# Kernel optimization log

Measured on AMD Instinct MI355X. Metric: run time of the kernel, lower is better.

## Reference

```python
import jax, jax.numpy as jnp
import numpy as np

N, E = 20000, 320000
IN_F, H, D = 1280, 4, 128
HD = H * D  # 512
NEG_SLOPE = 0.2


def setup_inputs() -> dict:
    key = jax.random.key(0)
    ks = jax.random.split(key, 16)
    feature = jax.random.normal(ks[0], (1, N, IN_F), dtype=jnp.float32)
    src = jax.random.randint(ks[1], (E,), 0, N, dtype=jnp.int32)
    dst = jnp.sort(jax.random.randint(ks[2], (E,), 0, N, dtype=jnp.int32))
    s1 = 1.0 / np.sqrt(IN_F)
    s2 = 1.0 / np.sqrt(HD)
    W1 = jax.random.normal(ks[3], (IN_F, HD), dtype=jnp.float32) * s1
    al1 = jax.random.normal(ks[4], (H, D), dtype=jnp.float32) * s2
    ar1 = jax.random.normal(ks[5], (H, D), dtype=jnp.float32) * s2
    b1 = jnp.zeros((HD,), dtype=jnp.float32)
    W2 = jax.random.normal(ks[6], (HD, HD), dtype=jnp.float32) * s2
    al2 = jax.random.normal(ks[7], (H, D), dtype=jnp.float32) * s2
    ar2 = jax.random.normal(ks[8], (H, D), dtype=jnp.float32) * s2
    b2 = jnp.zeros((HD,), dtype=jnp.float32)
    Wfc = jax.random.normal(ks[9], (HD, 64), dtype=jnp.float32) * s2
    bfc = jnp.zeros((64,), dtype=jnp.float32)
    return dict(feature=feature, src=src, dst=dst, W1=W1, al1=al1, ar1=ar1,
                b1=b1, W2=W2, al2=al2, ar2=ar2, b2=b2, Wfc=Wfc, bfc=bfc)


def gat_conv(x, src, dst, W, al, ar, b):
    # x: (N, F_in) -> (N, H, D). DGL GATConv math, negative_slope=0.2.
    h = (x @ W).reshape(N, H, D)
    el = jnp.sum(h * al, axis=-1)                       # (N, H)
    er = jnp.sum(h * ar, axis=-1)                       # (N, H)
    e = jax.nn.leaky_relu(el[src] + er[dst], NEG_SLOPE)  # (E, H)
    # edge softmax segmented by destination node
    m = jax.ops.segment_max(e, dst, num_segments=N, indices_are_sorted=True)
    ex = jnp.exp(e - m[dst])                            # (E, H)
    denom = jax.ops.segment_sum(ex, dst, num_segments=N, indices_are_sorted=True)
    alpha = ex / denom[dst]                             # (E, H)
    out = jax.ops.segment_sum(alpha[:, :, None] * h[src], dst,
                              num_segments=N, indices_are_sorted=True)  # (N,H,D)
    return out + b.reshape(H, D)


def reference(feature, src, dst, W1, al1, ar1, b1, W2, al2, ar2, b2, Wfc, bfc):
    x = feature[0]                                      # squeeze(0) -> (N, 1280)
    out = gat_conv(x, src, dst, W1, al1, ar1, b1)
    out = jax.nn.elu(out).reshape(N, HD)
    out = gat_conv(out, src, dst, W2, al2, ar2, b2)
    out = jax.nn.elu(out).reshape(N, HD)
    out = out @ Wfc + bfc                               # (N, 64)
    out = jax.nn.elu(out[None])                         # (1, N, 64)
    return out
```

## Files before the change

### kernel.cpp

```cpp
#include <hip/hip_runtime.h>
#include <hip/hip_bf16.h>
#include <math.h>
#include <type_traits>

typedef __bf16 bf16_t;
typedef __bf16 bf16x8 __attribute__((ext_vector_type(8)));
typedef float f32x4 __attribute__((ext_vector_type(4)));

__device__ __forceinline__ void gload_lds16(const void* g, void* l) {
  __builtin_amdgcn_global_load_lds((const __attribute__((address_space(1))) void*)g,
                                   (__attribute__((address_space(3))) void*)l, 16, 0, 0);
}

__global__ void transk(const float* __restrict__ in, bf16_t* __restrict__ out,
                       int K, int N) {
  __shared__ float t[32][33];
  int n0 = blockIdx.x * 32, k0 = blockIdx.y * 32;
  int tx = threadIdx.x & 31, ty = threadIdx.x >> 5;
#pragma unroll
  for (int r = ty; r < 32; r += 8) t[r][tx] = in[(size_t)(k0 + r) * N + n0 + tx];
  __syncthreads();
#pragma unroll
  for (int r = ty; r < 32; r += 8)
    out[(size_t)(n0 + r) * K + k0 + tx] = (bf16_t)t[tx][r];
}

__global__ void rowoffk(const int* __restrict__ dst, int* __restrict__ ro, int N, int E) {
  int n = blockIdx.x * blockDim.x + threadIdx.x;
  if (n > N) return;
  if (n == N) { ro[N] = E; return; }
  int lo = 0, hi = E;
  while (lo < hi) { int mid = (lo + hi) >> 1; if (dst[mid] < n) lo = mid + 1; else hi = mid; }
  ro[n] = lo;
}

__global__ void elerk(const bf16_t* __restrict__ Hb, const float* __restrict__ al,
                      const float* __restrict__ ar, float* __restrict__ el,
                      float* __restrict__ er, int N) {
  int node = blockIdx.x * 4 + (threadIdx.x >> 6);
  int lane = threadIdx.x & 63;
  if (node >= N) return;
  bf16x8 v = *(const bf16x8*)(Hb + (size_t)node * 512 + lane * 8);
  int head = lane >> 4;
  int dbase = (lane & 15) * 8;
  float sl = 0.f, sr = 0.f;
#pragma unroll
  for (int t = 0; t < 8; t++) {
    float f = (float)v[t];
    sl += f * al[head * 128 + dbase + t];
    sr += f * ar[head * 128 + dbase + t];
  }
#pragma unroll
  for (int off = 1; off < 16; off <<= 1) {
    sl += __shfl_xor(sl, off);
    sr += __shfl_xor(sr, off);
  }
  if ((lane & 15) == 0) {
    el[node * 4 + head] = sl;
    er[node * 4 + head] = sr;
  }
}

__global__ void edgek(const float* __restrict__ el, const float* __restrict__ er,
                      const int* __restrict__ src, const int* __restrict__ dst,
                      float* __restrict__ pw, int E) {
  int e = blockIdx.x * blockDim.x + threadIdx.x;
  if (e >= E) return;
  int s = src[e], d = dst[e];
  float4 ev = *(const float4*)(el + (size_t)s * 4);
  float4 rv = *(const float4*)(er + (size_t)d * 4);
  float c;
  c = ev.x + rv.x; c = c >= 0.f ? c : 0.2f * c; pw[e] = __expf(c);
  c = ev.y + rv.y; c = c >= 0.f ? c : 0.2f * c; pw[(size_t)E + e] = __expf(c);
  c = ev.z + rv.z; c = c >= 0.f ? c : 0.2f * c; pw[(size_t)2 * E + e] = __expf(c);
  c = ev.w + rv.w; c = c >= 0.f ? c : 0.2f * c; pw[(size_t)3 * E + e] = __expf(c);
}

#define GK_NPB 32
__global__ __launch_bounds__(256) void gatherk(
    const bf16_t* __restrict__ Hb, const float* __restrict__ pw,
    const int* __restrict__ src, const int* __restrict__ ro,
    const float* __restrict__ bias, bf16_t* __restrict__ out, int N, int E) {
  const int slice = blockIdx.x & 7;
  const int group = blockIdx.x >> 3;
  const int w = threadIdx.x >> 6, lane = threadIdx.x & 63;
  const int g = lane >> 3;
  const int oct = lane & 7;
  const int head = slice >> 1;
  const float* __restrict__ ph = pw + (size_t)head * E;
  const int dimbase = slice * 64 + oct * 8;

  const int n = group * GK_NPB + w * 8 + g;
  const int e0 = ro[n], e1 = ro[n + 1];

  float acc[8] = {0.f, 0.f, 0.f, 0.f, 0.f, 0.f, 0.f, 0.f};
  float psum = 0.f;

  for (int eb = e0 & ~7; eb < e1; eb += 8) {
    const int4 sv0 = *(const int4*)(src + eb);
    const int4 sv1 = *(const int4*)(src + eb + 4);
    const float4 pv0 = *(const float4*)(ph + eb);
    const float4 pv1 = *(const float4*)(ph + eb + 4);
    int ss[8]; float pp[8];
    ss[0] = sv0.x; ss[1] = sv0.y; ss[2] = sv0.z; ss[3] = sv0.w;
    ss[4] = sv1.x; ss[5] = sv1.y; ss[6] = sv1.z; ss[7] = sv1.w;
    pp[0] = pv0.x; pp[1] = pv0.y; pp[2] = pv0.z; pp[3] = pv0.w;
    pp[4] = pv1.x; pp[5] = pv1.y; pp[6] = pv1.z; pp[7] = pv1.w;
#pragma unroll
    for (int j = 0; j < 8; j++) {
      const int e = eb + j;
      if (e < e0 || e >= e1) pp[j] = 0.f;
    }
    bf16x8 v[8];
#pragma unroll
    for (int j = 0; j < 8; j++)
      v[j] = *(const bf16x8*)(Hb + (size_t)ss[j] * 512 + dimbase);
#pragma unroll
    for (int j = 0; j < 8; j++) {
      psum += pp[j];
#pragma unroll
      for (int t = 0; t < 8; t++) acc[t] += pp[j] * (float)v[j][t];
    }
  }

  const float ih = psum > 0.f ? 1.0f / psum : 0.f;
  const float4 b0 = *(const float4*)(bias + dimbase);
  const float4 b1 = *(const float4*)(bias + dimbase + 4);
  bf16x8 o; float vv;
  vv = acc[0] * ih + b0.x; o[0] = (bf16_t)(vv > 0.f ? vv : expm1f(vv));
  vv = acc[1] * ih + b0.y; o[1] = (bf16_t)(vv > 0.f ? vv : expm1f(vv));
  vv = acc[2] * ih + b0.z; o[2] = (bf16_t)(vv > 0.f ? vv : expm1f(vv));
  vv = acc[3] * ih + b0.w; o[3] = (bf16_t)(vv > 0.f ? vv : expm1f(vv));
  vv = acc[4] * ih + b1.x; o[4] = (bf16_t)(vv > 0.f ? vv : expm1f(vv));
  vv = acc[5] * ih + b1.y; o[5] = (bf16_t)(vv > 0.f ? vv : expm1f(vv));
  vv = acc[6] * ih + b1.z; o[6] = (bf16_t)(vv > 0.f ? vv : expm1f(vv));
  vv = acc[7] * ih + b1.w; o[7] = (bf16_t)(vv > 0.f ? vv : expm1f(vv));
  *(bf16x8*)(out + (size_t)n * 512 + dimbase) = o;
}

template <int BM, int BN, int WM, int WN, int EPI, int AF32>
__global__ __launch_bounds__(256) void gemm_bt(
    const void* __restrict__ A, const bf16_t* __restrict__ Bt,
    void* __restrict__ C, const float* __restrict__ bias,
    int M, int N, int K) {
  constexpr int BK = 32;
  constexpr int WTM = BM / WM, WTN = BN / WN;
  constexpr int MF = WTM / 16, NF = WTN / 16;
  using AT = typename std::conditional<AF32, float, bf16_t>::type;

  __shared__ AT sA[BM][BK];
  __shared__ bf16_t sB[BN][BK];

  const bf16_t* __restrict__ Ab = (const bf16_t*)A;
  const float* __restrict__ Af = (const float*)A;

  const int tid = threadIdx.x;
  const int wid = tid >> 6, lane = tid & 63;
  const int wr = wid / WN, wc = wid % WN;

  const int nby = N / BN;
  const int nwg = gridDim.x;
  const int q = nwg >> 3, r = nwg & 7;
  const int xcd = blockIdx.x & 7, pos = blockIdx.x >> 3;
  const int wg = (xcd < r ? xcd * (q + 1) : r * (q + 1) + (xcd - r) * q) + pos;
  const int row0 = (wg / nby) * BM;
  const int col0 = (wg % nby) * BN;

  f32x4 acc[MF][NF];
#pragma unroll
  for (int i = 0; i < MF; i++)
#pragma unroll
    for (int j = 0; j < NF; j++) acc[i][j] = (f32x4){0.f, 0.f, 0.f, 0.f};

  const int lr = lane >> 2;
  const int lkb = (lane & 3) * 8;
  const int a_lr = lane >> 3;
  const int a_seg = (lane & 7) ^ (lane >> 3);

  for (int k0 = 0; k0 < K; k0 += BK) {
    if constexpr (AF32) {
#pragma unroll
      for (int j = 0; j < BM / 32; j++) {
        const int rj = (j * 4 + wid) * 8;
        int grow = row0 + rj + a_lr; if (grow > M - 1) grow = M - 1;
        gload_lds16(Af + (size_t)grow * K + k0 + a_seg * 4, &sA[rj][0]);
      }
    } else {
#pragma unroll
      for (int i = 0; i < BM / 16; i += 4) {
        int r2 = (i + wid) * 16 + lr;
        int grow = row0 + r2; if (grow > M - 1) grow = M - 1;
        gload_lds16(Ab + (size_t)grow * K + k0 + lkb, &sA[(i + wid) * 16][0]);
      }
    }
#pragma unroll
    for (int i = 0; i < BN / 16; i += 4) {
      int r2 = (i + wid) * 16 + lr;
      gload_lds16(Bt + (size_t)(col0 + r2) * K + k0 + lkb, &sB[(i + wid) * 16][0]);
    }
    __syncthreads();
    bf16x8 af[MF], bfr[NF];
#pragma unroll
    for (int i = 0; i < MF; i++) {
      const int row = wr * WTM + i * 16 + (lane & 15);
      if constexpr (AF32) {
        const int h = lane >> 4;
        const int rowm = row & 7;
        const int p0 = (2 * h) ^ rowm, p1 = (2 * h + 1) ^ rowm;
        const f32x4 a0 = *(const f32x4*)&((const float*)&sA[row][0])[p0 * 4];
        const f32x4 a1 = *(const f32x4*)&((const float*)&sA[row][0])[p1 * 4];
#pragma unroll
        for (int t = 0; t < 4; t++) {
          af[i][t] = (bf16_t)a0[t];
          af[i][t + 4] = (bf16_t)a1[t];
        }
      } else {
        af[i] = *(const bf16x8*)&((const bf16_t*)&sA[row][0])[(lane >> 4) * 8];
      }
    }
#pragma unroll
    for (int j = 0; j < NF; j++)
      bfr[j] = *(const bf16x8*)&sB[wc * WTN + j * 16 + (lane & 15)][(lane >> 4) * 8];
#pragma unroll
    for (int i = 0; i < MF; i++)
#pragma unroll
      for (int j = 0; j < NF; j++)
        acc[i][j] = __builtin_amdgcn_mfma_f32_16x16x32_bf16(af[i], bfr[j], acc[i][j], 0, 0, 0);
    __syncthreads();
  }

#pragma unroll
  for (int i = 0; i < MF; i++) {
#pragma unroll
    for (int j = 0; j < NF; j++) {
#pragma unroll
      for (int rr = 0; rr < 4; rr++) {
        int row = row0 + wr * WTM + i * 16 + (lane >> 4) * 4 + rr;
        int col = col0 + wc * WTN + j * 16 + (lane & 15);
        if (row < M) {
          float v = acc[i][j][rr];
          if constexpr (EPI == 0) {
            ((bf16_t*)C)[(size_t)row * N + col] = (bf16_t)v;
          } else {
            v += bias[col];
            v = v > 0.f ? v : expm1f(v);
            ((float*)C)[(size_t)row * N + col] = v;
          }
        }
      }
    }
  }
}

extern "C" void kernel_launch(void* const* d_in, const int* in_sizes, int n_in,
                              void* d_out, int out_size, void* d_ws, size_t ws_size,
                              hipStream_t stream) {
  const float* feature = (const float*)d_in[0];
  const int* src = (const int*)d_in[1];
  const int* dst = (const int*)d_in[2];
  const float* W1 = (const float*)d_in[3];
  const float* al1 = (const float*)d_in[4];
  const float* ar1 = (const float*)d_in[5];
  const float* b1 = (const float*)d_in[6];
  const float* W2 = (const float*)d_in[7];
  const float* al2 = (const float*)d_in[8];
  const float* ar2 = (const float*)d_in[9];
  const float* b2 = (const float*)d_in[10];
  const float* Wfc = (const float*)d_in[11];
  const float* bfc = (const float*)d_in[12];

  const int N = 20000, E = 320000, INF = 1280, HD = 512;

  char* ws = (char*)d_ws;
  size_t off = 0;
  auto alloc = [&](size_t bytes) {
    void* p = ws + off;
    off += (bytes + 255) & ~(size_t)255;
    return p;
  };
  bf16_t* W1t = (bf16_t*)alloc((size_t)HD * INF * 2);
  bf16_t* W2t = (bf16_t*)alloc((size_t)HD * HD * 2);
  bf16_t* Wft = (bf16_t*)alloc((size_t)64 * HD * 2);
  bf16_t* Hb  = (bf16_t*)alloc((size_t)N * HD * 2);
  bf16_t* Xn  = (bf16_t*)alloc((size_t)N * HD * 2);
  float* el = (float*)alloc((size_t)N * 4 * 4);
  float* er = (float*)alloc((size_t)N * 4 * 4);
  float* pw = (float*)alloc((size_t)E * 4 * 4);
  int* ro = (int*)alloc((size_t)(N + 1) * 4);

  {
    dim3 g(HD / 32, INF / 32);
    transk<<<g, 256, 0, stream>>>(W1, W1t, INF, HD);
  }
  {
    dim3 g(HD / 32, HD / 32);
    transk<<<g, 256, 0, stream>>>(W2, W2t, HD, HD);
  }
  {
    dim3 g(64 / 32, HD / 32);
    transk<<<g, 256, 0, stream>>>(Wfc, Wft, HD, 64);
  }
  rowoffk<<<(N + 1 + 255) / 256, 256, 0, stream>>>(dst, ro, N, E);

  const int nbx = (N + 127) / 128;
  const int gatherBlocks = (N / GK_NPB) * 8;
  const int edgeBlocks = (E + 255) / 256;

  gemm_bt<128, 128, 2, 2, 0, 1><<<nbx * (HD / 128), 256, 0, stream>>>(
      feature, W1t, Hb, nullptr, N, HD, INF);
  elerk<<<N / 4, 256, 0, stream>>>(Hb, al1, ar1, el, er, N);
  edgek<<<edgeBlocks, 256, 0, stream>>>(el, er, src, dst, pw, E);
  gatherk<<<gatherBlocks, 256, 0, stream>>>(Hb, pw, src, ro, b1, Xn, N, E);

  gemm_bt<128, 128, 2, 2, 0, 0><<<nbx * (HD / 128), 256, 0, stream>>>(
      Xn, W2t, Hb, nullptr, N, HD, HD);
  elerk<<<N / 4, 256, 0, stream>>>(Hb, al2, ar2, el, er, N);
  edgek<<<edgeBlocks, 256, 0, stream>>>(el, er, src, dst, pw, E);
  gatherk<<<gatherBlocks, 256, 0, stream>>>(Hb, pw, src, ro, b2, Xn, N, E);

  gemm_bt<128, 64, 4, 1, 1, 0><<<nbx, 256, 0, stream>>>(Xn, Wft, d_out, bfc, N, 64, HD);
}
```

Baseline: 205.5 us.

## Add three-stage LDS multi-buffering with vmcnt waits to GEMM main loop

Turns the single-buffered GEMM K-loop into a three-stage software pipeline. Global-to-LDS loads for tile k+2 are issued while tile k is being computed, and a manual s_waitcnt vmcnt plus a single barrier per iteration replaces the two __syncthreads. This aims to hide global load latency behind the MFMA work. In exchange it triples LDS use, which may reduce occupancy, and it relies on exact vmcnt accounting; the tail iterations issue redundant clamped loads.

```diff
diff --git a/kernel.cpp b/kernel.cpp
--- a/kernel.cpp
+++ b/kernel.cpp
@@ -10,6 +10,20 @@
 __device__ __forceinline__ void gload_lds16(const void* g, void* l) {
   __builtin_amdgcn_global_load_lds((const __attribute__((address_space(1))) void*)g,
                                    (__attribute__((address_space(3))) void*)l, 16, 0, 0);
+}
+
+template <int N> __device__ __forceinline__ void wait_vm() {
+  static_assert(N >= 0 && N <= 12, "unsupported vmcnt");
+  if constexpr (N == 0)  asm volatile("s_waitcnt vmcnt(0)" ::: "memory");
+  else if constexpr (N == 1)  asm volatile("s_waitcnt vmcnt(1)" ::: "memory");
+  else if constexpr (N == 2)  asm volatile("s_waitcnt vmcnt(2)" ::: "memory");
+  else if constexpr (N == 3)  asm volatile("s_waitcnt vmcnt(3)" ::: "memory");
+  else if constexpr (N == 4)  asm volatile("s_waitcnt vmcnt(4)" ::: "memory");
+  else if constexpr (N == 5)  asm volatile("s_waitcnt vmcnt(5)" ::: "memory");
+  else if constexpr (N == 6)  asm volatile("s_waitcnt vmcnt(6)" ::: "memory");
+  else if constexpr (N == 7)  asm volatile("s_waitcnt vmcnt(7)" ::: "memory");
+  else if constexpr (N == 8)  asm volatile("s_waitcnt vmcnt(8)" ::: "memory");
+  else if constexpr (N == 12) asm volatile("s_waitcnt vmcnt(12)" ::: "memory");
 }
 
 __global__ void transk(const float* __restrict__ in, bf16_t* __restrict__ out,
@@ -144,12 +158,15 @@
     void* __restrict__ C, const float* __restrict__ bias,
     int M, int N, int K) {
   constexpr int BK = 32;
+  constexpr int S = 3;
   constexpr int WTM = BM / WM, WTN = BN / WN;
   constexpr int MF = WTM / 16, NF = WTN / 16;
+  constexpr int PER = (AF32 ? BM / 32 : BM / 64) + BN / 64;
+  constexpr int WAIT = (S - 2) * PER;
   using AT = typename std::conditional<AF32, float, bf16_t>::type;
 
-  __shared__ AT sA[BM][BK];
-  __shared__ bf16_t sB[BN][BK];
+  __shared__ AT sA[S][BM][BK];
+  __shared__ bf16_t sB[S][BN][BK];
 
   const bf16_t* __restrict__ Ab = (const bf16_t*)A;
   const float* __restrict__ Af = (const float*)A;
@@ -177,28 +194,43 @@
   const int a_lr = lane >> 3;
   const int a_seg = (lane & 7) ^ (lane >> 3);
 
-  for (int k0 = 0; k0 < K; k0 += BK) {
+  auto stage = [&](int st, int k0) {
     if constexpr (AF32) {
 #pragma unroll
       for (int j = 0; j < BM / 32; j++) {
         const int rj = (j * 4 + wid) * 8;
         int grow = row0 + rj + a_lr; if (grow > M - 1) grow = M - 1;
-        gload_lds16(Af + (size_t)grow * K + k0 + a_seg * 4, &sA[rj][0]);
+        gload_lds16(Af + (size_t)grow * K + k0 + a_seg * 4, &sA[st][rj][0]);
       }
     } else {
 #pragma unroll
       for (int i = 0; i < BM / 16; i += 4) {
         int r2 = (i + wid) * 16 + lr;
         int grow = row0 + r2; if (grow > M - 1) grow = M - 1;
-        gload_lds16(Ab + (size_t)grow * K + k0 + lkb, &sA[(i + wid) * 16][0]);
+        gload_lds16(Ab + (size_t)grow * K + k0 + lkb, &sA[st][(i + wid) * 16][0]);
       }
     }
 #pragma unroll
     for (int i = 0; i < BN / 16; i += 4) {
       int r2 = (i + wid) * 16 + lr;
-      gload_lds16(Bt + (size_t)(col0 + r2) * K + k0 + lkb, &sB[(i + wid) * 16][0]);
-    }
-    __syncthreads();
+      gload_lds16(Bt + (size_t)(col0 + r2) * K + k0 + lkb, &sB[st][(i + wid) * 16][0]);
+    }
+  };
+
+  const int NT = K / BK;
+#pragma unroll
+  for (int t = 0; t < S - 1; t++) stage(t, t * BK);
+
+  for (int k = 0; k < NT; k++) {
+    wait_vm<WAIT>();
+    __builtin_amdgcn_sched_barrier(0);
+    __builtin_amdgcn_s_barrier();
+    {
+      const int knext = k + S - 1;
+      const int tile = knext < NT ? knext : NT - 1;
+      stage(knext % S, tile * BK);
+    }
+    const int st = k % S;
     bf16x8 af[MF], bfr[NF];
 #pragma unroll
     for (int i = 0; i < MF; i++) {
@@ -207,26 +239,25 @@
         const int h = lane >> 4;
         const int rowm = row & 7;
         const int p0 = (2 * h) ^ rowm, p1 = (2 * h + 1) ^ rowm;
-        const f32x4 a0 = *(const f32x4*)&((const float*)&sA[row][0])[p0 * 4];
-        const f32x4 a1 = *(const f32x4*)&((const float*)&sA[row][0])[p1 * 4];
+        const f32x4 a0 = *(const f32x4*)&((const float*)&sA[st][row][0])[p0 * 4];
+        const f32x4 a1 = *(const f32x4*)&((const float*)&sA[st][row][0])[p1 * 4];
 #pragma unroll
         for (int t = 0; t < 4; t++) {
           af[i][t] = (bf16_t)a0[t];
           af[i][t + 4] = (bf16_t)a1[t];
         }
       } else {
-        af[i] = *(const bf16x8*)&((const bf16_t*)&sA[row][0])[(lane >> 4) * 8];
+        af[i] = *(const bf16x8*)&((const bf16_t*)&sA[st][row][0])[(lane >> 4) * 8];
       }
     }
 #pragma unroll
     for (int j = 0; j < NF; j++)
-      bfr[j] = *(const bf16x8*)&sB[wc * WTN + j * 16 + (lane & 15)][(lane >> 4) * 8];
+      bfr[j] = *(const bf16x8*)&sB[st][wc * WTN + j * 16 + (lane & 15)][(lane >> 4) * 8];
 #pragma unroll
     for (int i = 0; i < MF; i++)
 #pragma unroll
       for (int j = 0; j < NF; j++)
         acc[i][j] = __builtin_amdgcn_mfma_f32_16x16x32_bf16(af[i], bfr[j], acc[i][j], 0, 0, 0);
-    __syncthreads();
   }
 
 #pragma unroll
```

New measurement: 249.1 us. +21.2%, slower.
